# Kernel optimization log

Measured on AMD Instinct MI355X. Metric: run time of the kernel, lower is better.

Reference implementation:

```python
import jax, jax.numpy as jnp
import numpy as np

N, CS, CZ = 512, 384, 128
H, C, PQ, PV = 12, 16, 4, 8
NB = 8
EPS = 1e-8


def _ln(x, g, b):
    m = jnp.mean(x, axis=-1, keepdims=True)
    v = jnp.mean((x - m) ** 2, axis=-1, keepdims=True)
    return (x - m) / jnp.sqrt(v + 1e-5) * g + b


def _quat_rot(bcd):
    # (1, b, c, d) quaternion -> rotation matrix, as in AF2 BackboneUpdate
    ones = jnp.ones(bcd.shape[:-1] + (1,), bcd.dtype)
    q = jnp.concatenate([ones, bcd], axis=-1)
    q = q / jnp.linalg.norm(q, axis=-1, keepdims=True)
    w, x, y, z = q[..., 0], q[..., 1], q[..., 2], q[..., 3]
    R = jnp.stack([
        1 - 2 * (y * y + z * z), 2 * (x * y - w * z), 2 * (x * z + w * y),
        2 * (x * y + w * z), 1 - 2 * (x * x + z * z), 2 * (y * z - w * x),
        2 * (x * z - w * y), 2 * (y * z + w * x), 1 - 2 * (x * x + y * y),
    ], axis=-1)
    return R.reshape(bcd.shape[:-1] + (3, 3))


def _ipa(s, z, R, t, p):
    n = s.shape[0]
    q = (s @ p['w_q']).reshape(n, H, C)
    kv = (s @ p['w_kv']).reshape(n, H, 2, C)
    k, v = kv[..., 0, :], kv[..., 1, :]

    # local points -> global frames
    q_pts = (s @ p['w_qpts']).reshape(n, H * PQ, 3)
    q_pts = jnp.einsum('nxy,npy->npx', R, q_pts) + t[:, None, :]
    q_pts = q_pts.reshape(n, H, PQ, 3)
    kv_pts = (s @ p['w_kvpts']).reshape(n, H * (PQ + PV), 3)
    kv_pts = jnp.einsum('nxy,npy->npx', R, kv_pts) + t[:, None, :]
    kv_pts = kv_pts.reshape(n, H, PQ + PV, 3)
    k_pts, v_pts = kv_pts[:, :, :PQ], kv_pts[:, :, PQ:]

    b = z @ p['w_b']  # [i, j, H]

    scalar = jnp.einsum('ihc,jhc->hij', q, k) / np.sqrt(C)
    # sum_p ||q_ip - k_jp||^2 expanded to avoid [N,N,H,P,3] intermediate
    sq_q = jnp.sum(q_pts ** 2, axis=(-1, -2)).T  # [H, i]
    sq_k = jnp.sum(k_pts ** 2, axis=(-1, -2)).T  # [H, j]
    cross = jnp.einsum('ihpc,jhpc->hij', q_pts, k_pts)
    d2 = sq_q[:, :, None] + sq_k[:, None, :] - 2.0 * cross  # [H, i, j]

    gamma = jax.nn.softplus(p['head_weights'])  # [H]
    w_C = np.sqrt(2.0 / (9.0 * PQ))
    w_L = np.sqrt(1.0 / 3.0)
    logits = w_L * (scalar + jnp.transpose(b, (2, 0, 1))
                    - gamma[:, None, None] * (w_C / 2.0) * d2)
    a = jax.nn.softmax(logits, axis=-1)  # [H, i, j]

    o = jnp.einsum('hij,jhc->ihc', a, v).reshape(n, H * C)
    o_pt = jnp.einsum('hij,jhpc->ihpc', a, v_pts)
    # back to local frame: R_i^{-1} (o_pt - t_i)
    o_pt = jnp.einsum('nyx,nhpy->nhpx', R, o_pt - t[:, None, None, :])
    o_pt_norm = jnp.sqrt(jnp.sum(o_pt ** 2, axis=-1) + EPS)  # [n, H, PV]
    o_pair = jnp.einsum('hij,ijz->ihz', a, z).reshape(n, H * CZ)

    cat = jnp.concatenate([o, o_pt.reshape(n, H * PV * 3),
                           o_pt_norm.reshape(n, H * PV), o_pair], axis=-1)
    return cat @ p['w_out'] + p['b_out']


def _forward(s, z, p):
    n = s.shape[0]
    R = jnp.broadcast_to(jnp.eye(3, dtype=s.dtype), (n, 3, 3))
    t = jnp.zeros((n, 3), s.dtype)
    for _ in range(NB):  # shared weights across blocks, as in AF2
        s = s + _ipa(s, z, R, t, p)
        s = _ln(s, p['ln1_g'], p['ln1_b'])
        h = jax.nn.relu(s @ p['w_t1'])
        h = jax.nn.relu(h @ p['w_t2'])
        s = s + h @ p['w_t3']
        s = _ln(s, p['ln2_g'], p['ln2_b'])
        upd = s @ p['w_bb'] + p['b_bb']  # [n, 6]
        Ru = _quat_rot(upd[:, :3])
        tu = upd[:, 3:]
        t = jnp.einsum('nxy,ny->nx', R, tu) + t
        R = jnp.einsum('nxy,nyz->nxz', R, Ru)
    return jnp.concatenate([s, t], axis=-1)  # [n, CS + 3]


def setup_inputs() -> dict:
    key = jax.random.key(0)
    ks = jax.random.split(key, 12)
    sc = 0.02
    cat_dim = H * C + H * PV * 3 + H * PV + H * CZ  # 2112
    return {
        's': jax.random.normal(ks[0], (N, CS), jnp.float32),
        'z': jax.random.normal(ks[1], (N, N, CZ), jnp.float32),
        'w_q': jax.random.normal(ks[2], (CS, H * C), jnp.float32) * sc,
        'w_kv': jax.random.normal(ks[3], (CS, H * 2 * C), jnp.float32) * sc,
        'w_qpts': jax.random.normal(ks[4], (CS, H * PQ * 3), jnp.float32) * sc,
        'w_kvpts': jax.random.normal(ks[5], (CS, H * (PQ + PV) * 3), jnp.float32) * sc,
        'w_b': jax.random.normal(ks[6], (CZ, H), jnp.float32) * sc,
        'head_weights': jnp.zeros((H,), jnp.float32),
        'w_out': jax.random.normal(ks[7], (cat_dim, CS), jnp.float32) * sc,
        'b_out': jnp.zeros((CS,), jnp.float32),
        'ln1_g': jnp.ones((CS,), jnp.float32),
        'ln1_b': jnp.zeros((CS,), jnp.float32),
        'w_t1': jax.random.normal(ks[8], (CS, CS), jnp.float32) * sc,
        'w_t2': jax.random.normal(ks[9], (CS, CS), jnp.float32) * sc,
        'w_t3': jax.random.normal(ks[10], (CS, CS), jnp.float32) * sc,
        'ln2_g': jnp.ones((CS,), jnp.float32),
        'ln2_b': jnp.zeros((CS,), jnp.float32),
        'w_bb': jax.random.normal(ks[11], (CS, 6), jnp.float32) * sc,
        'b_bb': jnp.zeros((6,), jnp.float32),
    }


def reference(s, z, w_q, w_kv, w_qpts, w_kvpts, w_b, head_weights, w_out,
              b_out, ln1_g, ln1_b, w_t1, w_t2, w_t3, ln2_g, ln2_b, w_bb, b_bb):
    p = dict(w_q=w_q, w_kv=w_kv, w_qpts=w_qpts, w_kvpts=w_kvpts, w_b=w_b,
             head_weights=head_weights, w_out=w_out, b_out=b_out,
             ln1_g=ln1_g, ln1_b=ln1_b, w_t1=w_t1, w_t2=w_t2, w_t3=w_t3,
             ln2_g=ln2_g, ln2_b=ln2_b, w_bb=w_bb, b_bb=b_bb)
    return _forward(s, z, p)
```

## Files before the change

### kernel.cpp

```cpp
#include <hip/hip_runtime.h>
#include <hip/hip_bf16.h>

constexpr int Nres = 512;
constexpr int Cs   = 384;
constexpr int Cz   = 128;
constexpr int NH   = 12;
constexpr int HC   = 16;
constexpr int NPQ  = 4;
constexpr int NPV  = 8;
constexpr int NBLK = 8;
constexpr int PROJD = NH*HC + NH*2*HC + NH*NPQ*3 + NH*(NPQ+NPV)*3;
constexpr int CATD = NH*HC + NH*NPV*3 + NH*NPV + NH*Cz;
constexpr float W_L  = 0.57735026918962576f;
constexpr float W_C2 = 0.11785113019775793f;

using u16 = unsigned short;
typedef __bf16 bf16x8 __attribute__((ext_vector_type(8)));
typedef float  f32x4  __attribute__((ext_vector_type(4)));

static inline int gdiv(int n, int b) { return (n + b - 1) / b; }

static __device__ __forceinline__ u16 f2bf(float x) {
    __hip_bfloat16 h = __float2bfloat16(x);
    return *reinterpret_cast<u16*>(&h);
}
static __device__ __forceinline__ float bf2f(u16 x) {
    return __bfloat162float(*reinterpret_cast<__hip_bfloat16*>(&x));
}

__global__ void k_init(const float* __restrict__ s_in, float* __restrict__ s_cur,
                       u16* __restrict__ s_bf,
                       float* __restrict__ R, float* __restrict__ t) {
    int idx = blockIdx.x * blockDim.x + threadIdx.x;
    if (idx < Nres * Cs) { float v = s_in[idx]; s_cur[idx] = v; s_bf[idx] = f2bf(v); }
    if (idx < Nres * 9) {
        int e = idx % 9;
        R[idx] = (e == 0 || e == 4 || e == 8) ? 1.f : 0.f;
    }
    if (idx < Nres * 3) t[idx] = 0.f;
}

__global__ void k_concatW(const float* __restrict__ w_q, const float* __restrict__ w_kv,
                          const float* __restrict__ w_qpts, const float* __restrict__ w_kvpts,
                          float* __restrict__ Wcat) {
    int idx = blockIdx.x * blockDim.x + threadIdx.x;
    if (idx >= Cs * PROJD) return;
    int k = idx / PROJD, n = idx - k * PROJD;
    float v;
    if      (n < 192) v = w_q[k * 192 + n];
    else if (n < 576) v = w_kv[k * 384 + (n - 192)];
    else if (n < 720) v = w_qpts[k * 144 + (n - 576)];
    else              v = w_kvpts[k * 432 + (n - 720)];
    Wcat[idx] = v;
}

__global__ void k_transposeW(const float* __restrict__ in, u16* __restrict__ out,
                             int K, int N) {
    __shared__ float tile[32][33];
    int n0 = blockIdx.x * 32, k0 = blockIdx.y * 32;
    int tx = threadIdx.x & 31, ty = threadIdx.x >> 5;
#pragma unroll
    for (int j = 0; j < 4; j++)
        tile[ty + j * 8][tx] = in[(size_t)(k0 + ty + j * 8) * N + n0 + tx];
    __syncthreads();
#pragma unroll
    for (int j = 0; j < 4; j++)
        out[(size_t)(n0 + ty + j * 8) * K + k0 + tx] = f2bf(tile[tx][ty + j * 8]);
}

__global__ void k_zT(const float* __restrict__ z, u16* __restrict__ zT) {
    __shared__ float tile[32][33];
    int i  = blockIdx.x;
    int j0 = blockIdx.y * 32;
    int c0 = blockIdx.z * 32;
    int tx = threadIdx.x & 31, ty = threadIdx.x >> 5;
    const float* src = z + (size_t)i * Nres * Cz;
#pragma unroll
    for (int l = 0; l < 4; l++)
        tile[ty + l * 8][tx] = src[(size_t)(j0 + ty + l * 8) * Cz + c0 + tx];
    __syncthreads();
    u16* dst = zT + (size_t)i * Cz * Nres;
#pragma unroll
    for (int l = 0; l < 4; l++)
        dst[(size_t)(c0 + ty + l * 8) * Nres + j0 + tx] = f2bf(tile[tx][ty + l * 8]);
}

__global__ void __launch_bounds__(256)
k_gemm_mfma(const u16* __restrict__ A, const u16* __restrict__ Bt,
            float* __restrict__ P, int M, int K, int N, int Kc) {
    __shared__ u16 As[2][64 * 40];
    __shared__ u16 Bs[2][64 * 40];
    const int tid = threadIdx.x;
    const int m0 = blockIdx.y * 64;
    const int n0 = blockIdx.x * 64;
    const int kbeg = blockIdx.z * Kc;
    const int kend = kbeg + Kc;
    const int wv = tid >> 6, lane = tid & 63;
    const int wm = (wv >> 1) * 32, wn = (wv & 1) * 32;
    const int lrow = lane & 15, lq = lane >> 4;

    f32x4 zero = {0.f, 0.f, 0.f, 0.f};
    f32x4 acc00 = zero, acc01 = zero, acc10 = zero, acc11 = zero;

    const int srow = tid >> 2;
    const int sko  = (tid & 3) * 8;
    const size_t aoff = (size_t)(m0 + srow) * K + sko;
    const size_t boff = (size_t)(n0 + srow) * K + sko;

    uint4 ra = *(const uint4*)&A[aoff + kbeg];
    uint4 rb = *(const uint4*)&Bt[boff + kbeg];
    *(uint4*)&As[0][srow * 40 + sko] = ra;
    *(uint4*)&Bs[0][srow * 40 + sko] = rb;
    __syncthreads();

    int buf = 0;
    for (int k0 = kbeg; k0 < kend; k0 += 32) {
        const bool nxt = (k0 + 32 < kend);
        if (nxt) {
            ra = *(const uint4*)&A[aoff + k0 + 32];
            rb = *(const uint4*)&Bt[boff + k0 + 32];
        }
        bf16x8 a0 = *reinterpret_cast<const bf16x8*>(&As[buf][(wm + lrow) * 40 + lq * 8]);
        bf16x8 a1 = *reinterpret_cast<const bf16x8*>(&As[buf][(wm + 16 + lrow) * 40 + lq * 8]);
        bf16x8 b0 = *reinterpret_cast<const bf16x8*>(&Bs[buf][(wn + lrow) * 40 + lq * 8]);
        bf16x8 b1 = *reinterpret_cast<const bf16x8*>(&Bs[buf][(wn + 16 + lrow) * 40 + lq * 8]);
        acc00 = __builtin_amdgcn_mfma_f32_16x16x32_bf16(a0, b0, acc00, 0, 0, 0);
        acc01 = __builtin_amdgcn_mfma_f32_16x16x32_bf16(a0, b1, acc01, 0, 0, 0);
        acc10 = __builtin_amdgcn_mfma_f32_16x16x32_bf16(a1, b0, acc10, 0, 0, 0);
        acc11 = __builtin_amdgcn_mfma_f32_16x16x32_bf16(a1, b1, acc11, 0, 0, 0);
        if (nxt) {
            *(uint4*)&As[buf ^ 1][srow * 40 + sko] = ra;
            *(uint4*)&Bs[buf ^ 1][srow * 40 + sko] = rb;
            __syncthreads();
            buf ^= 1;
        }
    }
    float* Pp = P + (size_t)blockIdx.z * M * N;
    const int rbase = m0 + wm + lq * 4;
    const int cbase = n0 + wn + lrow;
#pragma unroll
    for (int r = 0; r < 4; r++) {
        Pp[(size_t)(rbase + r) * N + cbase]           = acc00[r];
        Pp[(size_t)(rbase + r) * N + cbase + 16]      = acc01[r];
        Pp[(size_t)(rbase + 16 + r) * N + cbase]      = acc10[r];
        Pp[(size_t)(rbase + 16 + r) * N + cbase + 16] = acc11[r];
    }
}

__global__ void __launch_bounds__(256)
k_gemm_rbf(const u16* __restrict__ A, const u16* __restrict__ Bt,
           float* __restrict__ outf, u16* __restrict__ outb,
           int M, int K, int N, int relu_bf) {
    __shared__ u16 As[2][32 * 40];
    __shared__ u16 Bs[2][64 * 40];
    const int tid = threadIdx.x;
    const int m0 = blockIdx.y * 32;
    const int n0 = blockIdx.x * 64;
    const int wv = tid >> 6, lane = tid & 63;
    const int wm = (wv >> 1) * 16, wn = (wv & 1) * 32;
    const int lrow = lane & 15, lq = lane >> 4;
    f32x4 zero = {0.f, 0.f, 0.f, 0.f};
    f32x4 acc0 = zero, acc1 = zero;
    const int srow = tid >> 2, sko = (tid & 3) * 8;
    const size_t aoff = (size_t)(m0 + srow) * K + sko;
    const size_t boff = (size_t)(n0 + srow) * K + sko;

    uint4 ra, rb;
    if (tid < 128) ra = *(const uint4*)&A[aoff];
    rb = *(const uint4*)&Bt[boff];
    if (tid < 128) *(uint4*)&As[0][srow * 40 + sko] = ra;
    *(uint4*)&Bs[0][srow * 40 + sko] = rb;
    __syncthreads();

    int buf = 0;
    for (int k0 = 0; k0 < K; k0 += 32) {
        const bool nxt = (k0 + 32 < K);
        if (nxt) {
            if (tid < 128) ra = *(const uint4*)&A[aoff + k0 + 32];
            rb = *(const uint4*)&Bt[boff + k0 + 32];
        }
        bf16x8 a  = *reinterpret_cast<const bf16x8*>(&As[buf][(wm + lrow) * 40 + lq * 8]);
        bf16x8 b0 = *reinterpret_cast<const bf16x8*>(&Bs[buf][(wn + lrow) * 40 + lq * 8]);
        bf16x8 b1 = *reinterpret_cast<const bf16x8*>(&Bs[buf][(wn + 16 + lrow) * 40 + lq * 8]);
        acc0 = __builtin_amdgcn_mfma_f32_16x16x32_bf16(a, b0, acc0, 0, 0, 0);
        acc1 = __builtin_amdgcn_mfma_f32_16x16x32_bf16(a, b1, acc1, 0, 0, 0);
        if (nxt) {
            if (tid < 128) *(uint4*)&As[buf ^ 1][srow * 40 + sko] = ra;
            *(uint4*)&Bs[buf ^ 1][srow * 40 + sko] = rb;
            __syncthreads();
            buf ^= 1;
        }
    }
    const int rbase = m0 + wm + lq * 4;
    const int cbase = n0 + wn + lrow;
    if (relu_bf) {
#pragma unroll
        for (int r = 0; r < 4; r++) {
            outb[(size_t)(rbase + r) * N + cbase]      = f2bf(fmaxf(acc0[r], 0.f));
            outb[(size_t)(rbase + r) * N + cbase + 16] = f2bf(fmaxf(acc1[r], 0.f));
        }
    } else {
#pragma unroll
        for (int r = 0; r < 4; r++) {
            outf[(size_t)(rbase + r) * N + cbase]      = acc0[r];
            outf[(size_t)(rbase + r) * N + cbase + 16] = acc1[r];
        }
    }
}

__global__ void k_bproj(const float* __restrict__ z, const float* __restrict__ w_b,
                        float* __restrict__ b_hij) {
    __shared__ float zs[16][129];
    __shared__ float wbs[Cz * NH];
    const int tid = threadIdx.x;
    const int base = blockIdx.x * 16;
#pragma unroll
    for (int l = 0; l < 6; l++) {
        int idx = tid + l * 256;
        if (idx < Cz * NH) wbs[idx] = w_b[idx];
    }
#pragma unroll
    for (int l = 0; l < 8; l++) {
        int idx = tid + l * 256;
        int r = idx >> 7, c = idx & 127;
        zs[r][c] = z[(size_t)(base + r) * Cz + c];
    }
    __syncthreads();
    if (tid < 192) {
        int h = tid >> 4, r = tid & 15;
        float acc = 0.f;
        for (int c = 0; c < Cz; c++) acc += zs[r][c] * wbs[c * NH + h];
        int row = base + r;
        int i = row >> 9, j = row & 511;
        b_hij[((size_t)h * Nres + i) * Nres + j] = acc * W_L;
    }
}

__global__ void k_prep(const float* __restrict__ proj, const float* __restrict__ R,
                       const float* __restrict__ t, const float* __restrict__ hw,
                       u16* __restrict__ Aaug, u16* __restrict__ Baug,
                       u16* __restrict__ vhT) {
    int idx = blockIdx.x * blockDim.x + threadIdx.x;
    if (idx >= NH * Nres) return;
    int h = idx / Nres, i = idx % Nres;
    float R_[9], t_[3];
#pragma unroll
    for (int e = 0; e < 9; e++) R_[e] = R[i * 9 + e];
#pragma unroll
    for (int e = 0; e < 3; e++) t_[e] = t[i * 3 + e];
    const float* prow = proj + (size_t)i * PROJD;
    float gam = log1pf(__expf(hw[h]));
    float ch  = sqrtf(2.f * gam * W_C2);

    u16 arow[32], brow[32];
#pragma unroll
    for (int c = 0; c < HC; c++) {
        arow[c] = f2bf(prow[h * HC + c] * (W_L * 0.25f));
        brow[c] = f2bf(prow[192 + h * 2 * HC + c]);
        vhT[((size_t)h * 48 + c) * Nres + i] = f2bf(prow[192 + h * 2 * HC + HC + c]);
    }
#pragma unroll
    for (int p = 0; p < NPQ; p++) {
        const float* src = prow + 576 + (h * NPQ + p) * 3;
        float y0 = src[0], y1 = src[1], y2 = src[2];
        float v0 = R_[0]*y0 + R_[1]*y1 + R_[2]*y2 + t_[0];
        float v1 = R_[3]*y0 + R_[4]*y1 + R_[5]*y2 + t_[1];
        float v2 = R_[6]*y0 + R_[7]*y1 + R_[8]*y2 + t_[2];
        float s = W_L * ch;
        arow[16 + p*3 + 0] = f2bf(v0 * s);
        arow[16 + p*3 + 1] = f2bf(v1 * s);
        arow[16 + p*3 + 2] = f2bf(v2 * s);
    }
    float sk = 0.f;
#pragma unroll
    for (int p = 0; p < NPQ + NPV; p++) {
        const float* src = prow + 720 + (h * (NPQ+NPV) + p) * 3;
        float y0 = src[0], y1 = src[1], y2 = src[2];
        float v0 = R_[0]*y0 + R_[1]*y1 + R_[2]*y2 + t_[0];
        float v1 = R_[3]*y0 + R_[4]*y1 + R_[5]*y2 + t_[1];
        float v2 = R_[6]*y0 + R_[7]*y1 + R_[8]*y2 + t_[2];
        if (p < NPQ) {
            brow[16 + p*3 + 0] = f2bf(v0 * ch);
            brow[16 + p*3 + 1] = f2bf(v1 * ch);
            brow[16 + p*3 + 2] = f2bf(v2 * ch);
            sk += v0*v0 + v1*v1 + v2*v2;
        } else {
            int c0 = 16 + (p - NPQ) * 3;
            vhT[((size_t)h * 48 + c0 + 0) * Nres + i] = f2bf(v0);
            vhT[((size_t)h * 48 + c0 + 1) * Nres + i] = f2bf(v1);
            vhT[((size_t)h * 48 + c0 + 2) * Nres + i] = f2bf(v2);
        }
    }
    float x = -W_L * gam * W_C2 * sk;
    u16 hi = f2bf(x);
    float lo = x - bf2f(hi);
    arow[28] = f2bf(1.0f); arow[29] = f2bf(1.0f); arow[30] = 0; arow[31] = 0;
    brow[28] = hi;         brow[29] = f2bf(lo);   brow[30] = 0; brow[31] = 0;

    uint4* ad = (uint4*)&Aaug[((size_t)h * Nres + i) * 32];
    uint4* bd = (uint4*)&Baug[((size_t)h * Nres + i) * 32];
    const uint4* as = (const uint4*)arow;
    const uint4* bs = (const uint4*)brow;
#pragma unroll
    for (int e = 0; e < 4; e++) { ad[e] = as[e]; bd[e] = bs[e]; }
}

__global__ void __launch_bounds__(256)
k_qk(const u16* __restrict__ Aaug, const u16* __restrict__ Baug,
     const float* __restrict__ b_hij, float* __restrict__ S) {
    __shared__ u16 As[64 * 40];
    __shared__ u16 Bs[64 * 40];
    const int tid = threadIdx.x;
    const int h  = blockIdx.z;
    const int i0 = blockIdx.y * 64;
    const int j0 = blockIdx.x * 64;
    const int wv = tid >> 6, lane = tid & 63;
    const int wm = (wv >> 1) * 32, wn = (wv & 1) * 32;
    const int lrow = lane & 15, lq = lane >> 4;
    const int srow = tid >> 2, sko = (tid & 3) * 8;

    *(uint4*)&As[srow * 40 + sko] = *(const uint4*)&Aaug[((size_t)h * Nres + i0 + srow) * 32 + sko];
    *(uint4*)&Bs[srow * 40 + sko] = *(const uint4*)&Baug[((size_t)h * Nres + j0 + srow) * 32 + sko];
    __syncthreads();

    f32x4 zero = {0.f, 0.f, 0.f, 0.f};
    bf16x8 a0 = *reinterpret_cast<const bf16x8*>(&As[(wm + lrow) * 40 + lq * 8]);
    bf16x8 a1 = *reinterpret_cast<const bf16x8*>(&As[(wm + 16 + lrow) * 40 + lq * 8]);
    bf16x8 b0 = *reinterpret_cast<const bf16x8*>(&Bs[(wn + lrow) * 40 + lq * 8]);
    bf16x8 b1 = *reinterpret_cast<const bf16x8*>(&Bs[(wn + 16 + lrow) * 40 + lq * 8]);
    f32x4 acc00 = __builtin_amdgcn_mfma_f32_16x16x32_bf16(a0, b0, zero, 0, 0, 0);
    f32x4 acc01 = __builtin_amdgcn_mfma_f32_16x16x32_bf16(a0, b1, zero, 0, 0, 0);
    f32x4 acc10 = __builtin_amdgcn_mfma_f32_16x16x32_bf16(a1, b0, zero, 0, 0, 0);
    f32x4 acc11 = __builtin_amdgcn_mfma_f32_16x16x32_bf16(a1, b1, zero, 0, 0, 0);

    const float* bh = b_hij + ((size_t)h * Nres + i0) * Nres + j0;
    float* Sp = S + ((size_t)h * Nres + i0) * Nres + j0;
    const int rbase = wm + lq * 4;
    const int cbase = wn + lrow;
#pragma unroll
    for (int r = 0; r < 4; r++) {
        Sp[(size_t)(rbase + r) * Nres + cbase]           = acc00[r] + bh[(size_t)(rbase + r) * Nres + cbase];
        Sp[(size_t)(rbase + r) * Nres + cbase + 16]      = acc01[r] + bh[(size_t)(rbase + r) * Nres + cbase + 16];
        Sp[(size_t)(rbase + 16 + r) * Nres + cbase]      = acc10[r] + bh[(size_t)(rbase + 16 + r) * Nres + cbase];
        Sp[(size_t)(rbase + 16 + r) * Nres + cbase + 16] = acc11[r] + bh[(size_t)(rbase + 16 + r) * Nres + cbase + 16];
    }
}

__global__ void __launch_bounds__(256)
k_sm_opair(const float* __restrict__ S, const u16* __restrict__ zT,
           u16* __restrict__ Pbf, u16* __restrict__ cat_bf) {
    __shared__ u16 P_lds[16 * 520];
    __shared__ u16 Bs[2][128 * 40];
    const int i = blockIdx.x;
    const int tid = threadIdx.x;
    const int wv = tid >> 6, ln = tid & 63;
    const int srow = tid >> 2, sko = (tid & 3) * 8;
    const u16* Bp = zT + (size_t)i * Cz * Nres;
    const size_t b0off = (size_t)srow * Nres + sko;
    const size_t b1off = (size_t)(64 + srow) * Nres + sko;

    uint4 rb0 = *(const uint4*)&Bp[b0off];
    uint4 rb1 = *(const uint4*)&Bp[b1off];

    for (int l = tid; l < 4 * 520; l += 256) P_lds[12 * 520 + l] = 0;

#pragma unroll
    for (int hh = 0; hh < 3; hh++) {
        int h = wv + hh * 4;
        const float* Srow = S + ((size_t)h * Nres + i) * Nres;
        float vals[8];
        float m = -1e30f;
#pragma unroll
        for (int jj = 0; jj < 8; jj++) { vals[jj] = Srow[ln + jj * 64]; m = fmaxf(m, vals[jj]); }
#pragma unroll
        for (int off = 32; off > 0; off >>= 1) m = fmaxf(m, __shfl_xor(m, off));
        float sm = 0.f;
#pragma unroll
        for (int jj = 0; jj < 8; jj++) { vals[jj] = __expf(vals[jj] - m); sm += vals[jj]; }
#pragma unroll
        for (int off = 32; off > 0; off >>= 1) sm += __shfl_xor(sm, off);
        float inv = 1.f / sm;
        u16* aP = Pbf + ((size_t)h * Nres + i) * Nres;
#pragma unroll
        for (int jj = 0; jj < 8; jj++) {
            u16 pb = f2bf(vals[jj] * inv);
            aP[ln + jj * 64] = pb;
            P_lds[h * 520 + ln + jj * 64] = pb;
        }
    }
    *(uint4*)&Bs[0][srow * 40 + sko]        = rb0;
    *(uint4*)&Bs[0][(64 + srow) * 40 + sko] = rb1;
    __syncthreads();

    const int lrow = ln & 15, lq = ln >> 4;
    const int wn = wv * 32;
    f32x4 zero = {0.f, 0.f, 0.f, 0.f};
    f32x4 acc0 = zero, acc1 = zero;
    int buf = 0;
    for (int k0 = 0; k0 < Nres; k0 += 32) {
        const bool nxt = (k0 + 32 < Nres);
        if (nxt) {
            rb0 = *(const uint4*)&Bp[b0off + k0 + 32];
            rb1 = *(const uint4*)&Bp[b1off + k0 + 32];
        }
        bf16x8 a  = *reinterpret_cast<const bf16x8*>(&P_lds[lrow * 520 + k0 + lq * 8]);
        bf16x8 b0 = *reinterpret_cast<const bf16x8*>(&Bs[buf][(wn + lrow) * 40 + lq * 8]);
        bf16x8 b1 = *reinterpret_cast<const bf16x8*>(&Bs[buf][(wn + 16 + lrow) * 40 + lq * 8]);
        acc0 = __builtin_amdgcn_mfma_f32_16x16x32_bf16(a, b0, acc0, 0, 0, 0);
        acc1 = __builtin_amdgcn_mfma_f32_16x16x32_bf16(a, b1, acc1, 0, 0, 0);
        if (nxt) {
            *(uint4*)&Bs[buf ^ 1][srow * 40 + sko]        = rb0;
            *(uint4*)&Bs[buf ^ 1][(64 + srow) * 40 + sko] = rb1;
            __syncthreads();
            buf ^= 1;
        }
    }
    u16* crow = cat_bf + (size_t)i * CATD + 576;
#pragma unroll
    for (int r = 0; r < 4; r++) {
        int row = lq * 4 + r;
        if (row < NH) {
            crow[row * Cz + wn + lrow]      = f2bf(acc0[r]);
            crow[row * Cz + wn + 16 + lrow] = f2bf(acc1[r]);
        }
    }
}

__global__ void __launch_bounds__(256)
k_ov(const u16* __restrict__ Pbf, const u16* __restrict__ vhT,
     const float* __restrict__ R, const float* __restrict__ t,
     u16* __restrict__ cat_bf) {
    __shared__ u16 As[2][64 * 40];
    __shared__ u16 Bs[2][48 * 40];
    __shared__ float Ct[64 * 49];
    const int h  = blockIdx.x;
    const int i0 = blockIdx.y * 64;
    const int tid = threadIdx.x;
    const int wv = tid >> 6, lane = tid & 63;
    const int lrow = lane & 15, lq = lane >> 4;
    const int wm = wv * 16;
    f32x4 zero = {0.f, 0.f, 0.f, 0.f};
    f32x4 acc0 = zero, acc1 = zero, acc2 = zero;
    const u16* Ap = Pbf + (size_t)h * Nres * Nres + (size_t)i0 * Nres;
    const u16* Bp = vhT + (size_t)h * 48 * Nres;
    const int srow = tid >> 2, sko = (tid & 3) * 8;
    const size_t aoff = (size_t)srow * Nres + sko;
    const size_t boff = (size_t)srow * Nres + sko;

    uint4 ra, rb;
    ra = *(const uint4*)&Ap[aoff];
    if (tid < 192) rb = *(const uint4*)&Bp[boff];
    *(uint4*)&As[0][srow * 40 + sko] = ra;
    if (tid < 192) *(uint4*)&Bs[0][srow * 40 + sko] = rb;
    __syncthreads();

    int buf = 0;
    for (int k0 = 0; k0 < Nres; k0 += 32) {
        const bool nxt = (k0 + 32 < Nres);
        if (nxt) {
            ra = *(const uint4*)&Ap[aoff + k0 + 32];
            if (tid < 192) rb = *(const uint4*)&Bp[boff + k0 + 32];
        }
        bf16x8 a  = *reinterpret_cast<const bf16x8*>(&As[buf][(wm + lrow) * 40 + lq * 8]);
        bf16x8 b0 = *reinterpret_cast<const bf16x8*>(&Bs[buf][(lrow) * 40 + lq * 8]);
        bf16x8 b1 = *reinterpret_cast<const bf16x8*>(&Bs[buf][(16 + lrow) * 40 + lq * 8]);
        bf16x8 b2 = *reinterpret_cast<const bf16x8*>(&Bs[buf][(32 + lrow) * 40 + lq * 8]);
        acc0 = __builtin_amdgcn_mfma_f32_16x16x32_bf16(a, b0, acc0, 0, 0, 0);
        acc1 = __builtin_amdgcn_mfma_f32_16x16x32_bf16(a, b1, acc1, 0, 0, 0);
        acc2 = __builtin_amdgcn_mfma_f32_16x16x32_bf16(a, b2, acc2, 0, 0, 0);
        if (nxt) {
            *(uint4*)&As[buf ^ 1][srow * 40 + sko] = ra;
            if (tid < 192) *(uint4*)&Bs[buf ^ 1][srow * 40 + sko] = rb;
            __syncthreads();
            buf ^= 1;
        }
    }
#pragma unroll
    for (int r = 0; r < 4; r++) {
        int row = wm + lq * 4 + r;
        Ct[row * 49 + lrow]      = acc0[r];
        Ct[row * 49 + 16 + lrow] = acc1[r];
        Ct[row * 49 + 32 + lrow] = acc2[r];
    }
    __syncthreads();
#pragma unroll
    for (int l = 0; l < 4; l++) {
        int idx = tid + l * 256;
        int r = idx >> 4, c = idx & 15;
        cat_bf[(size_t)(i0 + r) * CATD + h * HC + c] = f2bf(Ct[r * 49 + c]);
    }
#pragma unroll
    for (int l = 0; l < 2; l++) {
        int idx = tid + l * 256;
        int r = idx >> 3, p = idx & 7;
        int i = i0 + r;
        float g0 = Ct[r * 49 + 16 + p * 3 + 0];
        float g1 = Ct[r * 49 + 16 + p * 3 + 1];
        float g2 = Ct[r * 49 + 16 + p * 3 + 2];
        float d0 = g0 - t[i * 3 + 0], d1 = g1 - t[i * 3 + 1], d2v = g2 - t[i * 3 + 2];
        const float* Rn = R + i * 9;
        float l0 = Rn[0] * d0 + Rn[3] * d1 + Rn[6] * d2v;
        float l1 = Rn[1] * d0 + Rn[4] * d1 + Rn[7] * d2v;
        float l2 = Rn[2] * d0 + Rn[5] * d1 + Rn[8] * d2v;
        int hp = h * NPV + p;
        u16* crow = cat_bf + (size_t)i * CATD;
        crow[192 + hp * 3 + 0] = f2bf(l0);
        crow[192 + hp * 3 + 1] = f2bf(l1);
        crow[192 + hp * 3 + 2] = f2bf(l2);
        crow[480 + hp] = f2bf(sqrtf(l0 * l0 + l1 * l1 + l2 * l2 + 1e-8f));
    }
}

__global__ void k_reduce_ln(const float* __restrict__ P, const float* __restrict__ bias,
                            float* __restrict__ s, u16* __restrict__ s_bf,
                            const float* __restrict__ g, const float* __restrict__ b,
                            int nsplit) {
    __shared__ float red[512];
    int i = blockIdx.x, tid = threadIdx.x;
    float v = s[(size_t)i * Cs + tid];
    if (bias) v += bias[tid];
    for (int sp = 0; sp < nsplit; sp++) v += P[(size_t)sp * Nres * Cs + (size_t)i * Cs + tid];
    red[tid] = v;
    if (tid < 128) red[384 + tid] = 0.f;
    __syncthreads();
    for (int st = 256; st > 0; st >>= 1) { if (tid < st) red[tid] += red[tid + st]; __syncthreads(); }
    float mean = red[0] / Cs;
    __syncthreads();
    float d = v - mean;
    red[tid] = d * d;
    if (tid < 128) red[384 + tid] = 0.f;
    __syncthreads();
    for (int st = 256; st > 0; st >>= 1) { if (tid < st) red[tid] += red[tid + st]; __syncthreads(); }
    float var = red[0] / Cs;
    float o = d * rsqrtf(var + 1e-5f) * g[tid] + b[tid];
    s[(size_t)i * Cs + tid] = o;
    s_bf[(size_t)i * Cs + tid] = f2bf(o);
}

__global__ void k_reduce_ln_bb(const float* __restrict__ P, float* __restrict__ s,
                               u16* __restrict__ s_bf,
                               const float* __restrict__ g, const float* __restrict__ b,
                               int nsplit,
                               const float* __restrict__ w_bb, const float* __restrict__ b_bb,
                               float* __restrict__ R, float* __restrict__ t) {
    __shared__ float red[512];
    __shared__ float uw[36];
    int i = blockIdx.x, tid = threadIdx.x;
    float v = s[(size_t)i * Cs + tid];
    for (int sp = 0; sp < nsplit; sp++) v += P[(size_t)sp * Nres * Cs + (size_t)i * Cs + tid];
    red[tid] = v;
    if (tid < 128) red[384 + tid] = 0.f;
    __syncthreads();
    for (int st = 256; st > 0; st >>= 1) { if (tid < st) red[tid] += red[tid + st]; __syncthreads(); }
    float mean = red[0] / Cs;
    __syncthreads();
    float d = v - mean;
    red[tid] = d * d;
    if (tid < 128) red[384 + tid] = 0.f;
    __syncthreads();
    for (int st = 256; st > 0; st >>= 1) { if (tid < st) red[tid] += red[tid + st]; __syncthreads(); }
    float var = red[0] / Cs;
    float o = d * rsqrtf(var + 1e-5f) * g[tid] + b[tid];
    s[(size_t)i * Cs + tid] = o;
    s_bf[(size_t)i * Cs + tid] = f2bf(o);

    float u[6];
#pragma unroll
    for (int dd = 0; dd < 6; dd++) u[dd] = o * w_bb[tid * 6 + dd];
#pragma unroll
    for (int off = 32; off > 0; off >>= 1)
#pragma unroll
        for (int dd = 0; dd < 6; dd++) u[dd] += __shfl_xor(u[dd], off);
    int wv = tid >> 6, lane = tid & 63;
    if (lane == 0) {
#pragma unroll
        for (int dd = 0; dd < 6; dd++) uw[wv * 6 + dd] = u[dd];
    }
    __syncthreads();
    if (tid == 0) {
        float uu[6];
#pragma unroll
        for (int dd = 0; dd < 6; dd++) {
            float a = b_bb[dd];
            for (int w = 0; w < 6; w++) a += uw[w * 6 + dd];
            uu[dd] = a;
        }
        float qb = uu[0], qc = uu[1], qd = uu[2];
        float inv = rsqrtf(1.f + qb*qb + qc*qc + qd*qd);
        float w = inv, x = qb * inv, y = qc * inv, zq = qd * inv;
        float Ru[9] = {
            1.f - 2.f*(y*y + zq*zq), 2.f*(x*y - w*zq),       2.f*(x*zq + w*y),
            2.f*(x*y + w*zq),        1.f - 2.f*(x*x + zq*zq), 2.f*(y*zq - w*x),
            2.f*(x*zq - w*y),        2.f*(y*zq + w*x),        1.f - 2.f*(x*x + y*y)
        };
        float Ro[9];
#pragma unroll
        for (int e = 0; e < 9; e++) Ro[e] = R[i * 9 + e];
        float tu0 = uu[3], tu1 = uu[4], tu2 = uu[5];
        t[i*3+0] += Ro[0]*tu0 + Ro[1]*tu1 + Ro[2]*tu2;
        t[i*3+1] += Ro[3]*tu0 + Ro[4]*tu1 + Ro[5]*tu2;
        t[i*3+2] += Ro[6]*tu0 + Ro[7]*tu1 + Ro[8]*tu2;
#pragma unroll
        for (int r = 0; r < 3; r++)
#pragma unroll
            for (int c = 0; c < 3; c++)
                R[i*9 + r*3 + c] = Ro[r*3+0]*Ru[0*3+c] + Ro[r*3+1]*Ru[1*3+c] + Ro[r*3+2]*Ru[2*3+c];
    }
}

__global__ void k_final(const float* __restrict__ s, const float* __restrict__ t,
                        float* __restrict__ out) {
    int idx = blockIdx.x * blockDim.x + threadIdx.x;
    if (idx >= Nres * (Cs + 3)) return;
    int i = idx / (Cs + 3), c = idx - i * (Cs + 3);
    out[idx] = (c < Cs) ? s[(size_t)i * Cs + c] : t[i * 3 + (c - Cs)];
}

extern "C" void kernel_launch(void* const* d_in, const int* in_sizes, int n_in,
                              void* d_out, int out_size, void* d_ws, size_t ws_size,
                              hipStream_t stream) {
    const float* s_in    = (const float*)d_in[0];
    const float* z       = (const float*)d_in[1];
    const float* w_q     = (const float*)d_in[2];
    const float* w_kv    = (const float*)d_in[3];
    const float* w_qpts  = (const float*)d_in[4];
    const float* w_kvpts = (const float*)d_in[5];
    const float* w_b     = (const float*)d_in[6];
    const float* hw      = (const float*)d_in[7];
    const float* w_out   = (const float*)d_in[8];
    const float* b_out   = (const float*)d_in[9];
    const float* ln1_g   = (const float*)d_in[10];
    const float* ln1_b   = (const float*)d_in[11];
    const float* w_t1    = (const float*)d_in[12];
    const float* w_t2    = (const float*)d_in[13];
    const float* w_t3    = (const float*)d_in[14];
    const float* ln2_g   = (const float*)d_in[15];
    const float* ln2_b   = (const float*)d_in[16];
    const float* w_bb    = (const float*)d_in[17];
    const float* b_bb    = (const float*)d_in[18];
    float* out = (float*)d_out;

    float* ws = (float*)d_ws;
    size_t off = 0;
    float* s_cur = ws + off; off += (size_t)Nres * Cs;
    float* b_hij = ws + off; off += (size_t)NH * Nres * Nres;
    float* proj  = ws + off; off += (size_t)Nres * PROJD;
    float* Wcat  = ws + off; off += (size_t)Cs * PROJD;
    float* Rbuf  = ws + off; off += (size_t)Nres * 9;
    float* tbuf  = ws + off; off += (size_t)Nres * 3;
    float* Pslab = ws + off; off += (size_t)11 * Nres * Cs;
    float* Sbuf  = ws + off; off += (size_t)NH * Nres * Nres;
    u16* s_bf   = (u16*)(ws + off); off += (size_t)Nres * Cs / 2;
    u16* cat_bf = (u16*)(ws + off); off += (size_t)Nres * CATD / 2;
    u16* h1_bf  = (u16*)(ws + off); off += (size_t)Nres * Cs / 2;
    u16* h2_bf  = (u16*)(ws + off); off += (size_t)Nres * Cs / 2;
    u16* WcatT  = (u16*)(ws + off); off += (size_t)Cs * PROJD / 2;
    u16* w_outT = (u16*)(ws + off); off += (size_t)CATD * Cs / 2;
    u16* w_t1T  = (u16*)(ws + off); off += (size_t)Cs * Cs / 2;
    u16* w_t2T  = (u16*)(ws + off); off += (size_t)Cs * Cs / 2;
    u16* w_t3T  = (u16*)(ws + off); off += (size_t)Cs * Cs / 2;
    u16* Pbf    = (u16*)(ws + off); off += (size_t)NH * Nres * Nres / 2;
    u16* vhTbf  = (u16*)(ws + off); off += (size_t)NH * 48 * Nres / 2;
    u16* Aaug   = (u16*)(ws + off); off += (size_t)NH * Nres * 32 / 2;
    u16* Baug   = (u16*)(ws + off); off += (size_t)NH * Nres * 32 / 2;
    u16* zTbf   = (u16*)(ws + off); off += (size_t)Nres * Cz * Nres / 2;

    k_init<<<gdiv(Nres*Cs, 256), 256, 0, stream>>>(s_in, s_cur, s_bf, Rbuf, tbuf);
    k_concatW<<<gdiv(Cs*PROJD, 256), 256, 0, stream>>>(w_q, w_kv, w_qpts, w_kvpts, Wcat);
    k_transposeW<<<dim3(PROJD/32, Cs/32), 256, 0, stream>>>(Wcat, WcatT, Cs, PROJD);
    k_transposeW<<<dim3(Cs/32, CATD/32), 256, 0, stream>>>(w_out, w_outT, CATD, Cs);
    k_transposeW<<<dim3(Cs/32, Cs/32), 256, 0, stream>>>(w_t1, w_t1T, Cs, Cs);
    k_transposeW<<<dim3(Cs/32, Cs/32), 256, 0, stream>>>(w_t2, w_t2T, Cs, Cs);
    k_transposeW<<<dim3(Cs/32, Cs/32), 256, 0, stream>>>(w_t3, w_t3T, Cs, Cs);
    k_bproj<<<Nres*Nres/16, 256, 0, stream>>>(z, w_b, b_hij);
    k_zT<<<dim3(Nres, Nres/32, Cz/32), 256, 0, stream>>>(z, zTbf);

    for (int it = 0; it < NBLK; it++) {
        k_gemm_rbf<<<dim3(PROJD/64, Nres/32), 256, 0, stream>>>(s_bf, WcatT, proj, nullptr, Nres, Cs, PROJD, 0);
        k_prep<<<gdiv(NH*Nres, 256), 256, 0, stream>>>(proj, Rbuf, tbuf, hw, Aaug, Baug, vhTbf);
        k_qk<<<dim3(Nres/64, Nres/64, NH), 256, 0, stream>>>(Aaug, Baug, b_hij, Sbuf);
        k_sm_opair<<<Nres, 256, 0, stream>>>(Sbuf, zTbf, Pbf, cat_bf);
        k_ov<<<dim3(NH, Nres/64), 256, 0, stream>>>(Pbf, vhTbf, Rbuf, tbuf, cat_bf);
        k_gemm_mfma<<<dim3(Cs/64, Nres/64, 6), 256, 0, stream>>>(cat_bf, w_outT, Pslab, Nres, CATD, Cs, 352);
        k_reduce_ln<<<Nres, Cs, 0, stream>>>(Pslab, b_out, s_cur, s_bf, ln1_g, ln1_b, 6);
        k_gemm_rbf<<<dim3(Cs/64, Nres/32), 256, 0, stream>>>(s_bf, w_t1T, nullptr, h1_bf, Nres, Cs, Cs, 1);
        k_gemm_rbf<<<dim3(Cs/64, Nres/32), 256, 0, stream>>>(h1_bf, w_t2T, nullptr, h2_bf, Nres, Cs, Cs, 1);
        k_gemm_rbf<<<dim3(Cs/64, Nres/32), 256, 0, stream>>>(h2_bf, w_t3T, Pslab, nullptr, Nres, Cs, Cs, 0);
        k_reduce_ln_bb<<<Nres, Cs, 0, stream>>>(Pslab, s_cur, s_bf, ln2_g, ln2_b, 1, w_bb, b_bb, Rbuf, tbuf);
    }

    k_final<<<gdiv(Nres*(Cs+3), 256), 256, 0, stream>>>(s_cur, tbuf, out);
}
```

Measured before the change: 948.3 us.

## Fuse QK logits, softmax and PV into one attention kernel per head tile

Merges the QK score kernel, the row softmax and the attention-times-values kernel into a single k_attn kernel. Each block computes a full 64x512 logit tile in registers, applies softmax, and keeps the bf16 probabilities in LDS for the PV product. This removes the fp32 score buffer round trip through global memory and one kernel launch. The pair-feature product moves to a separate k_opair kernel that reads the stored bf16 probabilities. The cost is fewer blocks (96), a large per-thread accumulator array (32 f32x4) that raises register pressure, and a larger LDS footprint.

Measured after the change: 919.5 us. -3.0%, faster.

```diff
diff --git a/kernel.cpp b/kernel.cpp
--- a/kernel.cpp
+++ b/kernel.cpp
@@ -306,171 +306,115 @@
 }
 
 __global__ void __launch_bounds__(256)
-k_qk(const u16* __restrict__ Aaug, const u16* __restrict__ Baug,
-     const float* __restrict__ b_hij, float* __restrict__ S) {
-    __shared__ u16 As[64 * 40];
-    __shared__ u16 Bs[64 * 40];
-    const int tid = threadIdx.x;
-    const int h  = blockIdx.z;
-    const int i0 = blockIdx.y * 64;
-    const int j0 = blockIdx.x * 64;
-    const int wv = tid >> 6, lane = tid & 63;
-    const int wm = (wv >> 1) * 32, wn = (wv & 1) * 32;
-    const int lrow = lane & 15, lq = lane >> 4;
-    const int srow = tid >> 2, sko = (tid & 3) * 8;
-
-    *(uint4*)&As[srow * 40 + sko] = *(const uint4*)&Aaug[((size_t)h * Nres + i0 + srow) * 32 + sko];
-    *(uint4*)&Bs[srow * 40 + sko] = *(const uint4*)&Baug[((size_t)h * Nres + j0 + srow) * 32 + sko];
-    __syncthreads();
-
-    f32x4 zero = {0.f, 0.f, 0.f, 0.f};
-    bf16x8 a0 = *reinterpret_cast<const bf16x8*>(&As[(wm + lrow) * 40 + lq * 8]);
-    bf16x8 a1 = *reinterpret_cast<const bf16x8*>(&As[(wm + 16 + lrow) * 40 + lq * 8]);
-    bf16x8 b0 = *reinterpret_cast<const bf16x8*>(&Bs[(wn + lrow) * 40 + lq * 8]);
-    bf16x8 b1 = *reinterpret_cast<const bf16x8*>(&Bs[(wn + 16 + lrow) * 40 + lq * 8]);
-    f32x4 acc00 = __builtin_amdgcn_mfma_f32_16x16x32_bf16(a0, b0, zero, 0, 0, 0);
-    f32x4 acc01 = __builtin_amdgcn_mfma_f32_16x16x32_bf16(a0, b1, zero, 0, 0, 0);
-    f32x4 acc10 = __builtin_amdgcn_mfma_f32_16x16x32_bf16(a1, b0, zero, 0, 0, 0);
-    f32x4 acc11 = __builtin_amdgcn_mfma_f32_16x16x32_bf16(a1, b1, zero, 0, 0, 0);
-
-    const float* bh = b_hij + ((size_t)h * Nres + i0) * Nres + j0;
-    float* Sp = S + ((size_t)h * Nres + i0) * Nres + j0;
-    const int rbase = wm + lq * 4;
-    const int cbase = wn + lrow;
-#pragma unroll
-    for (int r = 0; r < 4; r++) {
-        Sp[(size_t)(rbase + r) * Nres + cbase]           = acc00[r] + bh[(size_t)(rbase + r) * Nres + cbase];
-        Sp[(size_t)(rbase + r) * Nres + cbase + 16]      = acc01[r] + bh[(size_t)(rbase + r) * Nres + cbase + 16];
-        Sp[(size_t)(rbase + 16 + r) * Nres + cbase]      = acc10[r] + bh[(size_t)(rbase + 16 + r) * Nres + cbase];
-        Sp[(size_t)(rbase + 16 + r) * Nres + cbase + 16] = acc11[r] + bh[(size_t)(rbase + 16 + r) * Nres + cbase + 16];
-    }
-}
-
-__global__ void __launch_bounds__(256)
-k_sm_opair(const float* __restrict__ S, const u16* __restrict__ zT,
-           u16* __restrict__ Pbf, u16* __restrict__ cat_bf) {
-    __shared__ u16 P_lds[16 * 520];
-    __shared__ u16 Bs[2][128 * 40];
-    const int i = blockIdx.x;
-    const int tid = threadIdx.x;
-    const int wv = tid >> 6, ln = tid & 63;
-    const int srow = tid >> 2, sko = (tid & 3) * 8;
-    const u16* Bp = zT + (size_t)i * Cz * Nres;
-    const size_t b0off = (size_t)srow * Nres + sko;
-    const size_t b1off = (size_t)(64 + srow) * Nres + sko;
-
-    uint4 rb0 = *(const uint4*)&Bp[b0off];
-    uint4 rb1 = *(const uint4*)&Bp[b1off];
-
-    for (int l = tid; l < 4 * 520; l += 256) P_lds[12 * 520 + l] = 0;
-
-#pragma unroll
-    for (int hh = 0; hh < 3; hh++) {
-        int h = wv + hh * 4;
-        const float* Srow = S + ((size_t)h * Nres + i) * Nres;
-        float vals[8];
-        float m = -1e30f;
-#pragma unroll
-        for (int jj = 0; jj < 8; jj++) { vals[jj] = Srow[ln + jj * 64]; m = fmaxf(m, vals[jj]); }
-#pragma unroll
-        for (int off = 32; off > 0; off >>= 1) m = fmaxf(m, __shfl_xor(m, off));
-        float sm = 0.f;
-#pragma unroll
-        for (int jj = 0; jj < 8; jj++) { vals[jj] = __expf(vals[jj] - m); sm += vals[jj]; }
-#pragma unroll
-        for (int off = 32; off > 0; off >>= 1) sm += __shfl_xor(sm, off);
-        float inv = 1.f / sm;
-        u16* aP = Pbf + ((size_t)h * Nres + i) * Nres;
-#pragma unroll
-        for (int jj = 0; jj < 8; jj++) {
-            u16 pb = f2bf(vals[jj] * inv);
-            aP[ln + jj * 64] = pb;
-            P_lds[h * 520 + ln + jj * 64] = pb;
-        }
-    }
-    *(uint4*)&Bs[0][srow * 40 + sko]        = rb0;
-    *(uint4*)&Bs[0][(64 + srow) * 40 + sko] = rb1;
-    __syncthreads();
-
-    const int lrow = ln & 15, lq = ln >> 4;
-    const int wn = wv * 32;
-    f32x4 zero = {0.f, 0.f, 0.f, 0.f};
-    f32x4 acc0 = zero, acc1 = zero;
-    int buf = 0;
-    for (int k0 = 0; k0 < Nres; k0 += 32) {
-        const bool nxt = (k0 + 32 < Nres);
-        if (nxt) {
-            rb0 = *(const uint4*)&Bp[b0off + k0 + 32];
-            rb1 = *(const uint4*)&Bp[b1off + k0 + 32];
-        }
-        bf16x8 a  = *reinterpret_cast<const bf16x8*>(&P_lds[lrow * 520 + k0 + lq * 8]);
-        bf16x8 b0 = *reinterpret_cast<const bf16x8*>(&Bs[buf][(wn + lrow) * 40 + lq * 8]);
-        bf16x8 b1 = *reinterpret_cast<const bf16x8*>(&Bs[buf][(wn + 16 + lrow) * 40 + lq * 8]);
-        acc0 = __builtin_amdgcn_mfma_f32_16x16x32_bf16(a, b0, acc0, 0, 0, 0);
-        acc1 = __builtin_amdgcn_mfma_f32_16x16x32_bf16(a, b1, acc1, 0, 0, 0);
-        if (nxt) {
-            *(uint4*)&Bs[buf ^ 1][srow * 40 + sko]        = rb0;
-            *(uint4*)&Bs[buf ^ 1][(64 + srow) * 40 + sko] = rb1;
-            __syncthreads();
-            buf ^= 1;
-        }
-    }
-    u16* crow = cat_bf + (size_t)i * CATD + 576;
-#pragma unroll
-    for (int r = 0; r < 4; r++) {
-        int row = lq * 4 + r;
-        if (row < NH) {
-            crow[row * Cz + wn + lrow]      = f2bf(acc0[r]);
-            crow[row * Cz + wn + 16 + lrow] = f2bf(acc1[r]);
-        }
-    }
-}
-
-__global__ void __launch_bounds__(256)
-k_ov(const u16* __restrict__ Pbf, const u16* __restrict__ vhT,
-     const float* __restrict__ R, const float* __restrict__ t,
-     u16* __restrict__ cat_bf) {
-    __shared__ u16 As[2][64 * 40];
-    __shared__ u16 Bs[2][48 * 40];
+k_attn(const u16* __restrict__ Aaug, const u16* __restrict__ Baug,
+       const float* __restrict__ b_hij, const u16* __restrict__ vhT,
+       const float* __restrict__ R, const float* __restrict__ t,
+       u16* __restrict__ Pbf, u16* __restrict__ cat_bf) {
+    __shared__ union {
+        struct { u16 A[64 * 40]; u16 B[512 * 40]; } qk;
+        u16 P[64 * 520];
+    } U;
+    __shared__ u16 Bsv[2][48 * 40];
     __shared__ float Ct[64 * 49];
-    const int h  = blockIdx.x;
-    const int i0 = blockIdx.y * 64;
+
+    const int i0 = blockIdx.x * 64;
+    const int h  = blockIdx.y;
     const int tid = threadIdx.x;
     const int wv = tid >> 6, lane = tid & 63;
     const int lrow = lane & 15, lq = lane >> 4;
     const int wm = wv * 16;
+    const int srow = tid >> 2, sko = (tid & 3) * 8;
+
+    const u16* Bp = vhT + (size_t)h * 48 * Nres;
+    const size_t boff = (size_t)srow * Nres + sko;
+    if (tid < 192) {
+        uint4 rv = *(const uint4*)&Bp[boff];
+        *(uint4*)&Bsv[0][srow * 40 + sko] = rv;
+    }
+
+    {
+        int r4 = tid >> 2, q = tid & 3;
+        *(uint4*)&U.qk.A[r4 * 40 + q * 8] =
+            *(const uint4*)&Aaug[((size_t)h * Nres + i0 + r4) * 32 + q * 8];
+#pragma unroll
+        for (int l = 0; l < 8; l++) {
+            int idx = tid + l * 256;
+            int rr = idx >> 2, qq = idx & 3;
+            *(uint4*)&U.qk.B[rr * 40 + qq * 8] =
+                *(const uint4*)&Baug[((size_t)h * Nres + rr) * 32 + qq * 8];
+        }
+    }
+    __syncthreads();
+
     f32x4 zero = {0.f, 0.f, 0.f, 0.f};
-    f32x4 acc0 = zero, acc1 = zero, acc2 = zero;
-    const u16* Ap = Pbf + (size_t)h * Nres * Nres + (size_t)i0 * Nres;
-    const u16* Bp = vhT + (size_t)h * 48 * Nres;
-    const int srow = tid >> 2, sko = (tid & 3) * 8;
-    const size_t aoff = (size_t)srow * Nres + sko;
-    const size_t boff = (size_t)srow * Nres + sko;
-
-    uint4 ra, rb;
-    ra = *(const uint4*)&Ap[aoff];
-    if (tid < 192) rb = *(const uint4*)&Bp[boff];
-    *(uint4*)&As[0][srow * 40 + sko] = ra;
-    if (tid < 192) *(uint4*)&Bs[0][srow * 40 + sko] = rb;
-    __syncthreads();
-
+    bf16x8 afrag = *reinterpret_cast<const bf16x8*>(&U.qk.A[(wm + lrow) * 40 + lq * 8]);
+    f32x4 acc[32];
+#pragma unroll
+    for (int tt = 0; tt < 32; tt++) {
+        bf16x8 bfr = *reinterpret_cast<const bf16x8*>(&U.qk.B[(tt * 16 + lrow) * 40 + lq * 8]);
+        acc[tt] = __builtin_amdgcn_mfma_f32_16x16x32_bf16(afrag, bfr, zero, 0, 0, 0);
+    }
+    const float* bh = b_hij + ((size_t)h * Nres + (i0 + wm + lq * 4)) * Nres;
+#pragma unroll
+    for (int tt = 0; tt < 32; tt++) {
+#pragma unroll
+        for (int r = 0; r < 4; r++)
+            acc[tt][r] += bh[(size_t)r * Nres + tt * 16 + lrow];
+    }
+    float mx[4] = {-1e30f, -1e30f, -1e30f, -1e30f};
+#pragma unroll
+    for (int tt = 0; tt < 32; tt++)
+#pragma unroll
+        for (int r = 0; r < 4; r++) mx[r] = fmaxf(mx[r], acc[tt][r]);
+#pragma unroll
+    for (int off = 8; off > 0; off >>= 1)
+#pragma unroll
+        for (int r = 0; r < 4; r++) mx[r] = fmaxf(mx[r], __shfl_xor(mx[r], off));
+    float sm[4] = {0.f, 0.f, 0.f, 0.f};
+#pragma unroll
+    for (int tt = 0; tt < 32; tt++)
+#pragma unroll
+        for (int r = 0; r < 4; r++) { acc[tt][r] = __expf(acc[tt][r] - mx[r]); sm[r] += acc[tt][r]; }
+#pragma unroll
+    for (int off = 8; off > 0; off >>= 1)
+#pragma unroll
+        for (int r = 0; r < 4; r++) sm[r] += __shfl_xor(sm[r], off);
+    float inv[4];
+#pragma unroll
+    for (int r = 0; r < 4; r++) inv[r] = 1.f / sm[r];
+
+    __syncthreads();
+
+#pragma unroll
+    for (int tt = 0; tt < 32; tt++)
+#pragma unroll
+        for (int r = 0; r < 4; r++)
+            U.P[(wm + lq * 4 + r) * 520 + tt * 16 + lrow] = f2bf(acc[tt][r] * inv[r]);
+    __syncthreads();
+
+#pragma unroll
+    for (int l = 0; l < 16; l++) {
+        int v = tid + l * 256;
+        int rr = v >> 6, cq = v & 63;
+        *(uint4*)&Pbf[((size_t)h * Nres + i0 + rr) * 512 + cq * 8] =
+            *(const uint4*)&U.P[rr * 520 + cq * 8];
+    }
+
+    f32x4 o0 = zero, o1 = zero, o2 = zero;
     int buf = 0;
     for (int k0 = 0; k0 < Nres; k0 += 32) {
         const bool nxt = (k0 + 32 < Nres);
+        uint4 rv;
+        if (nxt && tid < 192) rv = *(const uint4*)&Bp[boff + k0 + 32];
+        bf16x8 a  = *reinterpret_cast<const bf16x8*>(&U.P[(wm + lrow) * 520 + k0 + lq * 8]);
+        bf16x8 b0 = *reinterpret_cast<const bf16x8*>(&Bsv[buf][(lrow) * 40 + lq * 8]);
+        bf16x8 b1 = *reinterpret_cast<const bf16x8*>(&Bsv[buf][(16 + lrow) * 40 + lq * 8]);
+        bf16x8 b2 = *reinterpret_cast<const bf16x8*>(&Bsv[buf][(32 + lrow) * 40 + lq * 8]);
+        o0 = __builtin_amdgcn_mfma_f32_16x16x32_bf16(a, b0, o0, 0, 0, 0);
+        o1 = __builtin_amdgcn_mfma_f32_16x16x32_bf16(a, b1, o1, 0, 0, 0);
+        o2 = __builtin_amdgcn_mfma_f32_16x16x32_bf16(a, b2, o2, 0, 0, 0);
         if (nxt) {
-            ra = *(const uint4*)&Ap[aoff + k0 + 32];
-            if (tid < 192) rb = *(const uint4*)&Bp[boff + k0 + 32];
-        }
-        bf16x8 a  = *reinterpret_cast<const bf16x8*>(&As[buf][(wm + lrow) * 40 + lq * 8]);
-        bf16x8 b0 = *reinterpret_cast<const bf16x8*>(&Bs[buf][(lrow) * 40 + lq * 8]);
-        bf16x8 b1 = *reinterpret_cast<const bf16x8*>(&Bs[buf][(16 + lrow) * 40 + lq * 8]);
-        bf16x8 b2 = *reinterpret_cast<const bf16x8*>(&Bs[buf][(32 + lrow) * 40 + lq * 8]);
-        acc0 = __builtin_amdgcn_mfma_f32_16x16x32_bf16(a, b0, acc0, 0, 0, 0);
-        acc1 = __builtin_amdgcn_mfma_f32_16x16x32_bf16(a, b1, acc1, 0, 0, 0);
-        acc2 = __builtin_amdgcn_mfma_f32_16x16x32_bf16(a, b2, acc2, 0, 0, 0);
-        if (nxt) {
-            *(uint4*)&As[buf ^ 1][srow * 40 + sko] = ra;
-            if (tid < 192) *(uint4*)&Bs[buf ^ 1][srow * 40 + sko] = rb;
+            if (tid < 192) *(uint4*)&Bsv[buf ^ 1][srow * 40 + sko] = rv;
             __syncthreads();
             buf ^= 1;
         }
@@ -478,9 +422,9 @@
 #pragma unroll
     for (int r = 0; r < 4; r++) {
         int row = wm + lq * 4 + r;
-        Ct[row * 49 + lrow]      = acc0[r];
-        Ct[row * 49 + 16 + lrow] = acc1[r];
-        Ct[row * 49 + 32 + lrow] = acc2[r];
+        Ct[row * 49 + lrow]      = o0[r];
+        Ct[row * 49 + 16 + lrow] = o1[r];
+        Ct[row * 49 + 32 + lrow] = o2[r];
     }
     __syncthreads();
 #pragma unroll
@@ -508,6 +452,69 @@
         crow[192 + hp * 3 + 1] = f2bf(l1);
         crow[192 + hp * 3 + 2] = f2bf(l2);
         crow[480 + hp] = f2bf(sqrtf(l0 * l0 + l1 * l1 + l2 * l2 + 1e-8f));
+    }
+}
+
+__global__ void __launch_bounds__(256)
+k_opair(const u16* __restrict__ Pbf, const u16* __restrict__ zT,
+        u16* __restrict__ cat_bf) {
+    __shared__ u16 P_lds[16 * 520];
+    __shared__ u16 Bs[2][128 * 40];
+    const int i = blockIdx.x;
+    const int tid = threadIdx.x;
+    const int wv = tid >> 6, ln = tid & 63;
+    const int srow = tid >> 2, sko = (tid & 3) * 8;
+    const u16* Bp = zT + (size_t)i * Cz * Nres;
+    const size_t b0off = (size_t)srow * Nres + sko;
+    const size_t b1off = (size_t)(64 + srow) * Nres + sko;
+
+    uint4 rb0 = *(const uint4*)&Bp[b0off];
+    uint4 rb1 = *(const uint4*)&Bp[b1off];
+
+#pragma unroll
+    for (int l = 0; l < 3; l++) {
+        int v = tid + l * 256;
+        int hh = v >> 6, cq = v & 63;
+        *(uint4*)&P_lds[hh * 520 + cq * 8] =
+            *(const uint4*)&Pbf[((size_t)hh * Nres + i) * 512 + cq * 8];
+    }
+    for (int l = tid; l < 4 * 520; l += 256) P_lds[12 * 520 + l] = 0;
+
+    *(uint4*)&Bs[0][srow * 40 + sko]        = rb0;
+    *(uint4*)&Bs[0][(64 + srow) * 40 + sko] = rb1;
+    __syncthreads();
+
+    const int lrow = ln & 15, lq = ln >> 4;
+    const int wn = wv * 32;
+    f32x4 zero = {0.f, 0.f, 0.f, 0.f};
+    f32x4 acc0 = zero, acc1 = zero;
+    int buf = 0;
+    for (int k0 = 0; k0 < Nres; k0 += 32) {
+        const bool nxt = (k0 + 32 < Nres);
+        if (nxt) {
+            rb0 = *(const uint4*)&Bp[b0off + k0 + 32];
+            rb1 = *(const uint4*)&Bp[b1off + k0 + 32];
+        }
+        bf16x8 a  = *reinterpret_cast<const bf16x8*>(&P_lds[lrow * 520 + k0 + lq * 8]);
+        bf16x8 b0 = *reinterpret_cast<const bf16x8*>(&Bs[buf][(wn + lrow) * 40 + lq * 8]);
+        bf16x8 b1 = *reinterpret_cast<const bf16x8*>(&Bs[buf][(wn + 16 + lrow) * 40 + lq * 8]);
+        acc0 = __builtin_amdgcn_mfma_f32_16x16x32_bf16(a, b0, acc0, 0, 0, 0);
+        acc1 = __builtin_amdgcn_mfma_f32_16x16x32_bf16(a, b1, acc1, 0, 0, 0);
+        if (nxt) {
+            *(uint4*)&Bs[buf ^ 1][srow * 40 + sko]        = rb0;
+            *(uint4*)&Bs[buf ^ 1][(64 + srow) * 40 + sko] = rb1;
+            __syncthreads();
+            buf ^= 1;
+        }
+    }
+    u16* crow = cat_bf + (size_t)i * CATD + 576;
+#pragma unroll
+    for (int r = 0; r < 4; r++) {
+        int row = lq * 4 + r;
+        if (row < NH) {
+            crow[row * Cz + wn + lrow]      = f2bf(acc0[r]);
+            crow[row * Cz + wn + 16 + lrow] = f2bf(acc1[r]);
+        }
     }
 }
 
@@ -649,7 +656,6 @@
     float* Rbuf  = ws + off; off += (size_t)Nres * 9;
     float* tbuf  = ws + off; off += (size_t)Nres * 3;
     float* Pslab = ws + off; off += (size_t)11 * Nres * Cs;
-    float* Sbuf  = ws + off; off += (size_t)NH * Nres * Nres;
     u16* s_bf   = (u16*)(ws + off); off += (size_t)Nres * Cs / 2;
     u16* cat_bf = (u16*)(ws + off); off += (size_t)Nres * CATD / 2;
     u16* h1_bf  = (u16*)(ws + off); off += (size_t)Nres * Cs / 2;
@@ -678,9 +684,8 @@
     for (int it = 0; it < NBLK; it++) {
         k_gemm_rbf<<<dim3(PROJD/64, Nres/32), 256, 0, stream>>>(s_bf, WcatT, proj, nullptr, Nres, Cs, PROJD, 0);
         k_prep<<<gdiv(NH*Nres, 256), 256, 0, stream>>>(proj, Rbuf, tbuf, hw, Aaug, Baug, vhTbf);
-        k_qk<<<dim3(Nres/64, Nres/64, NH), 256, 0, stream>>>(Aaug, Baug, b_hij, Sbuf);
-        k_sm_opair<<<Nres, 256, 0, stream>>>(Sbuf, zTbf, Pbf, cat_bf);
-        k_ov<<<dim3(NH, Nres/64), 256, 0, stream>>>(Pbf, vhTbf, Rbuf, tbuf, cat_bf);
+        k_attn<<<dim3(Nres/64, NH), 256, 0, stream>>>(Aaug, Baug, b_hij, vhTbf, Rbuf, tbuf, Pbf, cat_bf);
+        k_opair<<<Nres, 256, 0, stream>>>(Pbf, zTbf, cat_bf);
         k_gemm_mfma<<<dim3(Cs/64, Nres/64, 6), 256, 0, stream>>>(cat_bf, w_outT, Pslab, Nres, CATD, Cs, 352);
         k_reduce_ln<<<Nres, Cs, 0, stream>>>(Pslab, b_out, s_cur, s_bf, ln1_g, ln1_b, 6);
         k_gemm_rbf<<<dim3(Cs/64, Nres/32), 256, 0, stream>>>(s_bf, w_t1T, nullptr, h1_bf, Nres, Cs, Cs, 1);
```
